# Kernel optimization log

Hardware: AMD Instinct MI355X
Metric: run time of the kernel (lower is better)

Reference implementation:

```python
import jax, jax.numpy as jnp
import numpy as np

B, L, D, H = 32, 512, 256, 4
A = 64
DH = D // H   # 64, item/pos head dim
AH = A // H   # 16, attribute head dim
EPS = 1e-12


def _split(t, h):
    # [B, L, d] -> [B, h, L, d//h]
    b, l, d = t.shape
    return t.reshape(b, l, h, d // h).transpose(0, 2, 1, 3)


def setup_inputs() -> dict:
    key = jax.random.key(0)
    ks = jax.random.split(key, 16)
    n = lambda k, s, sc=1.0: jax.random.normal(k, s, dtype=jnp.float32) * sc
    W = 0.02  # weight init scale
    return {
        "x": n(ks[0], (B, L, D)),
        "pos": n(ks[1], (B, L, D)),
        "true_item": n(ks[2], (B, L, D)),
        "attr0": n(ks[3], (B, L, 1, A)),
        "attr1": n(ks[4], (B, L, 1, A)),
        "mask": jnp.zeros((1, 1, L, L), jnp.float32),
        "Wq": n(ks[5], (D, D), W), "bq": jnp.zeros((D,), jnp.float32),
        "Wk": n(ks[6], (D, D), W), "bk": jnp.zeros((D,), jnp.float32),
        "Wqp": n(ks[7], (D, D), W), "bqp": jnp.zeros((D,), jnp.float32),
        "Wkp": n(ks[8], (D, D), W), "bkp": jnp.zeros((D,), jnp.float32),
        "Wq0": n(ks[9], (A, A), W), "bq0": jnp.zeros((A,), jnp.float32),
        "Wk0": n(ks[10], (A, A), W), "bk0": jnp.zeros((A,), jnp.float32),
        "Wq1": n(ks[11], (A, A), W), "bq1": jnp.zeros((A,), jnp.float32),
        "Wk1": n(ks[12], (A, A), W), "bk1": jnp.zeros((A,), jnp.float32),
        "Wd": n(ks[13], (D, D), W), "bd": jnp.zeros((D,), jnp.float32),
        "ln_g": jnp.ones((D,), jnp.float32),
        "ln_b": jnp.zeros((D,), jnp.float32),
    }


def reference(x, pos, true_item, attr0, attr1, mask,
              Wq, bq, Wk, bk, Wqp, bqp, Wkp, bkp,
              Wq0, bq0, Wk0, bk0, Wq1, bq1, Wk1, bk1,
              Wd, bd, ln_g, ln_b):
    lin = lambda t, W, b: t @ W + b
    # item / positional / attribute projections
    q = _split(lin(x, Wq, bq), H)           # [B,H,L,DH]
    k = _split(lin(x, Wk, bk), H)
    v = _split(true_item, H)                # value = true_item directly (no value proj in forward)
    qp = _split(lin(pos, Wqp, bqp), H)
    kp = _split(lin(pos, Wkp, bkp), H)
    a0 = attr0[:, :, 0, :]                  # squeeze(-2) -> [B,L,A]
    a1 = attr1[:, :, 0, :]
    q0 = _split(lin(a0, Wq0, bq0), H)       # [B,H,L,AH]
    k0 = _split(lin(a0, Wk0, bk0), H)
    q1 = _split(lin(a1, Wq1, bq1), H)
    k1 = _split(lin(a1, Wk1, bk1), H)
    # fused multi-source score accumulation (fusion_type='sum')
    scores = (jnp.einsum('bhld,bhmd->bhlm', q, k)
              + jnp.einsum('bhld,bhmd->bhlm', qp, kp)
              + jnp.einsum('bhld,bhmd->bhlm', q0, k0)
              + jnp.einsum('bhld,bhmd->bhlm', q1, k1))
    scores = scores / np.float32(np.sqrt(DH)) + mask
    probs = jax.nn.softmax(scores, axis=-1)  # attn_dropout p=0 -> identity
    ctx = jnp.einsum('bhlm,bhmd->bhld', probs, v)
    ctx = ctx.transpose(0, 2, 1, 3).reshape(B, L, D)
    h = lin(ctx, Wd, bd)                     # out_dropout p=0 -> identity
    mu = h.mean(-1, keepdims=True)
    var = h.var(-1, keepdims=True)
    return ln_g * (h - mu) / jnp.sqrt(var + EPS) + ln_b + x
```

## Files before the change

### kernel.cpp

```cpp
#include <hip/hip_runtime.h>

typedef unsigned short u16;
typedef unsigned int u32;

#define BB 32
#define LL 512
#define DD 256
#define HH 4
#define CAT 160
#define MTOT (BB*LL)

typedef __bf16 bf16x8 __attribute__((ext_vector_type(8)));
typedef float f32x4 __attribute__((ext_vector_type(4)));

__device__ __forceinline__ float b2f(u16 u) {
  union { u32 i; float f; } v; v.i = ((u32)u) << 16; return v.f;
}
__device__ __forceinline__ u16 f2b(float f) {
  union { float f; u32 i; } v; v.f = f;
  u32 x = v.i;
  u32 r = (x + 0x7FFFu + ((x >> 16) & 1u)) >> 16;
  return (u16)r;
}

template<bool F32>
__device__ __forceinline__ float ldin(const void* p, size_t i) {
  if constexpr (F32) return ((const float*)p)[i];
  else return b2f(((const u16*)p)[i]);
}

__device__ __forceinline__ bool f32mode(const void* lng) {
  return ((const u16*)lng)[0] == 0;
}

__device__ __forceinline__ f32x4 mfma_bf16(uint4 a, uint4 b, f32x4 c) {
  union U { uint4 u; bf16x8 v; };
  U ua, ub; ua.u = a; ub.u = b;
  return __builtin_amdgcn_mfma_f32_16x16x32_bf16(ua.v, ub.v, c, 0, 0, 0);
}

template<bool F32>
__device__ __forceinline__ void ld8(const void* p, size_t g, u16* tmp) {
  if constexpr (F32) {
    const float* gp = (const float*)p + g;
    float4 x0 = *(const float4*)gp;
    float4 x1 = *(const float4*)(gp + 4);
    tmp[0] = f2b(x0.x); tmp[1] = f2b(x0.y); tmp[2] = f2b(x0.z); tmp[3] = f2b(x0.w);
    tmp[4] = f2b(x1.x); tmp[5] = f2b(x1.y); tmp[6] = f2b(x1.z); tmp[7] = f2b(x1.w);
  } else {
    *(uint4*)tmp = *(const uint4*)((const u16*)p + g);
  }
}

struct WtOp { const void* W; u16* dst; int N; int K; };
struct WtArgs { WtOp ops[8]; const void* lng; };

template<bool F32>
__device__ void wtrans_body(const WtArgs& args, u16* T ) {
  WtOp op = args.ops[blockIdx.z];
  const int ntN = op.N >> 6;
  const int tx = blockIdx.x % ntN;
  const int ty = blockIdx.x / ntN;
  if (ty >= (op.K >> 6)) return;
  const int n0 = tx * 64, k0 = ty * 64;
  const int tid = threadIdx.x;
  for (int i = tid; i < 512; i += 256) {
    int r = i >> 3, c8 = (i & 7) * 8;
    u16 tmp[8];
    ld8<F32>(op.W, (size_t)(k0 + r) * op.N + n0 + c8, tmp);
    *(uint4*)&T[r * 72 + c8] = *(uint4*)tmp;
  }
  __syncthreads();
  for (int i = tid; i < 512; i += 256) {
    int n = i >> 3, k8 = (i & 7) * 8;
    u16 tmp[8];
#pragma unroll
    for (int j = 0; j < 8; ++j) tmp[j] = T[(k8 + j) * 72 + n];
    *(uint4*)(op.dst + (size_t)(n0 + n) * op.K + k0 + k8) = *(uint4*)tmp;
  }
}

__global__ __launch_bounds__(256) void wtrans_kernel(WtArgs args) {
  __shared__ __align__(16) u16 smem[64 * 72];
  if (f32mode(args.lng)) wtrans_body<true>(args, smem);
  else wtrans_body<false>(args, smem);
}

struct ProjOp {
  const void* X; const u16* Wt; const void* bias; u16* dst;
  int N; int K; int dstOff; int hShift; int dMask;
};
struct ProjArgs { ProjOp ops[8]; const void* lng; };

template<bool F32>
__device__ void proj_body(const ProjArgs& args, u16* smem) {
  ProjOp op = args.ops[blockIdx.z];
  const int n0g = blockIdx.y * 64;
  if (n0g >= op.N) return;
  const int m0 = blockIdx.x * 64;
  const int K = op.K;
  const int tid = threadIdx.x;
  const int wave = tid >> 6, lane = tid & 63;
  const int quad = lane >> 4, l15 = lane & 15;

  u16* Xs = smem;
  u16* Wt = smem + 64 * 136;

  f32x4 acc[4];
#pragma unroll
  for (int c = 0; c < 4; ++c) acc[c] = (f32x4){0.f, 0.f, 0.f, 0.f};

  for (int kc = 0; kc < K; kc += 128) {
    const int kw = (K - kc < 128) ? (K - kc) : 128;
    const int kw8 = kw >> 3;
    __syncthreads();
    for (int i = tid; i < 64 * kw8; i += 256) {
      int r = i / kw8, c8 = (i % kw8) * 8;
      u16 tmp[8];
      ld8<F32>(op.X, (size_t)(m0 + r) * K + kc + c8, tmp);
      *(uint4*)&Xs[r * 136 + c8] = *(uint4*)tmp;
    }
    for (int i = tid; i < 64 * kw8; i += 256) {
      int r = i / kw8, c8 = (i % kw8) * 8;
      *(uint4*)&Wt[r * 136 + c8] =
          *(const uint4*)(op.Wt + (size_t)(n0g + r) * K + kc + c8);
    }
    __syncthreads();
    const int nks = kw >> 5;
    for (int ks = 0; ks < nks; ++ks) {
      uint4 a = *(const uint4*)&Xs[(wave * 16 + l15) * 136 + ks * 32 + quad * 8];
#pragma unroll
      for (int c = 0; c < 4; ++c) {
        uint4 bb = *(const uint4*)&Wt[(c * 16 + l15) * 136 + ks * 32 + quad * 8];
        acc[c] = mfma_bf16(a, bb, acc[c]);
      }
    }
  }
  const int mrow = m0 + wave * 16 + quad * 4;
#pragma unroll
  for (int c = 0; c < 4; ++c) {
    int n = n0g + c * 16 + l15;
    int h = n >> op.hShift, d = n & op.dMask;
    float bias = ldin<F32>(op.bias, n);
#pragma unroll
    for (int r4 = 0; r4 < 4; ++r4) {
      int m = mrow + r4;
      int b = m >> 9, l = m & 511;
      op.dst[(size_t)((b * HH + h) * LL + l) * CAT + op.dstOff + d] =
          f2b(acc[c][r4] + bias);
    }
  }
}

__global__ __launch_bounds__(256) void proj_kernel(ProjArgs args) {
  __shared__ __align__(16) u16 smem[2 * 64 * 136];
  if (f32mode(args.lng)) proj_body<true>(args, smem);
  else proj_body<false>(args, smem);
}

template<bool F32>
__device__ void attn_body(
    const u16* __restrict__ qcat, const u16* __restrict__ kcat,
    const void* __restrict__ titm, const void* __restrict__ mask,
    float* __restrict__ ctx, u16* smem) {
  const int tid = threadIdx.x;
  const int wave = tid >> 6, lane = tid & 63;
  const int quad = lane >> 4, l15 = lane & 15;
  const int bh = blockIdx.x, b = bh >> 2, h = bh & 3;
  const int q0g = blockIdx.y * 64;

  u16* Ks = smem;
  u16* Vt = smem + 64 * 168;
  u16* Pw = smem + 64 * 168 + 64 * 72;

  for (int i = tid; i < 1280; i += 256) {
    int r = i / 20, c = (i % 20) * 8;
    *(uint4*)&Ks[r * 168 + c] =
        *(const uint4*)(qcat + (size_t)(bh * LL + q0g + r) * CAT + c);
  }
  __syncthreads();
  uint4 aq[5];
#pragma unroll
  for (int ks = 0; ks < 5; ++ks)
    aq[ks] = *(const uint4*)&Ks[(wave * 16 + l15) * 168 + ks * 32 + quad * 8];

  float lsum[4] = {0.f, 0.f, 0.f, 0.f};
  f32x4 oa[4];
#pragma unroll
  for (int vt = 0; vt < 4; ++vt) oa[vt] = (f32x4){0.f, 0.f, 0.f, 0.f};

  for (int c = 0; c < 8; ++c) {
    __syncthreads();
    for (int i = tid; i < 1280; i += 256) {
      int r = i / 20, col = (i % 20) * 8;
      *(uint4*)&Ks[r * 168 + col] =
          *(const uint4*)(kcat + (size_t)(bh * LL + c * 64 + r) * CAT + col);
    }
    for (int i = tid; i < 512; i += 256) {
      int t8 = i & 7, key = i >> 3;
      u16 tmp[8];
      ld8<F32>(titm, (size_t)(b * LL + c * 64 + key) * DD + h * 64 + t8 * 8, tmp);
#pragma unroll
      for (int j = 0; j < 8; ++j) Vt[(t8 * 8 + j) * 72 + key] = tmp[j];
    }
    __syncthreads();

    f32x4 s[4];
#pragma unroll
    for (int ct = 0; ct < 4; ++ct) {
      s[ct] = (f32x4){0.f, 0.f, 0.f, 0.f};
#pragma unroll
      for (int ks = 0; ks < 5; ++ks) {
        uint4 bk = *(const uint4*)&Ks[(ct * 16 + l15) * 168 + ks * 32 + quad * 8];
        s[ct] = mfma_bf16(aq[ks], bk, s[ct]);
      }
    }
#pragma unroll
    for (int ct = 0; ct < 4; ++ct) {
      int key = c * 64 + ct * 16 + l15;
#pragma unroll
      for (int r4 = 0; r4 < 4; ++r4) {
        int row = q0g + wave * 16 + quad * 4 + r4;
        float e = __expf(s[ct][r4] * 0.125f +
                         ldin<F32>(mask, (size_t)row * LL + key));
        lsum[r4] += e;
        Pw[wave * 16 * 72 + (quad * 4 + r4) * 72 + ct * 16 + l15] = f2b(e);
      }
    }
#pragma unroll
    for (int ks2 = 0; ks2 < 2; ++ks2) {
      uint4 pa = *(const uint4*)&Pw[wave * 16 * 72 + l15 * 72 + ks2 * 32 + quad * 8];
#pragma unroll
      for (int vt = 0; vt < 4; ++vt) {
        uint4 bb = *(const uint4*)&Vt[(vt * 16 + l15) * 72 + ks2 * 32 + quad * 8];
        oa[vt] = mfma_bf16(pa, bb, oa[vt]);
      }
    }
  }
  float inv[4];
#pragma unroll
  for (int r4 = 0; r4 < 4; ++r4) {
    for (int off = 1; off < 16; off <<= 1)
      lsum[r4] += __shfl_xor(lsum[r4], off);
    inv[r4] = 1.0f / lsum[r4];
  }
#pragma unroll
  for (int vt = 0; vt < 4; ++vt)
#pragma unroll
    for (int r4 = 0; r4 < 4; ++r4) {
      int row = q0g + wave * 16 + quad * 4 + r4;
      ctx[(size_t)(b * LL + row) * DD + h * 64 + vt * 16 + l15] =
          oa[vt][r4] * inv[r4];
    }
}

__global__ __launch_bounds__(256) void attn_kernel(
    const u16* __restrict__ qcat, const u16* __restrict__ kcat,
    const void* __restrict__ titm, const void* __restrict__ mask,
    float* __restrict__ ctx, const void* lng) {
  __shared__ __align__(16) u16 smem[64 * 168 + 64 * 72 + 4 * 16 * 72];
  if (f32mode(lng)) attn_body<true>(qcat, kcat, titm, mask, ctx, smem);
  else attn_body<false>(qcat, kcat, titm, mask, ctx, smem);
}

template<bool F32>
__device__ void outln_body(
    const float* __restrict__ ctx, const void* __restrict__ Wd,
    const void* __restrict__ bd, const void* __restrict__ ln_g,
    const void* __restrict__ ln_b, const void* __restrict__ x,
    float* __restrict__ out, float* smem) {
  const int tid = threadIdx.x;
  const int row0 = blockIdx.x * 8;
  float (*ctxs)[260] = (float (*)[260])smem;
  float* mu_s = smem + 8 * 260;
  float* rs_s = mu_s + 8;
  for (int i = tid; i < 8 * 256; i += 256) {
    int r = i >> 8, k = i & 255;
    ctxs[r][k] = ctx[(size_t)(row0 + r) * DD + k];
  }
  __syncthreads();
  const int n = tid;
  float acc[8];
  float bias = ldin<F32>(bd, n);
#pragma unroll
  for (int r = 0; r < 8; ++r) acc[r] = bias;
  for (int k4 = 0; k4 < 256; k4 += 4) {
    float w0 = ldin<F32>(Wd, (size_t)(k4 + 0) * DD + n);
    float w1 = ldin<F32>(Wd, (size_t)(k4 + 1) * DD + n);
    float w2 = ldin<F32>(Wd, (size_t)(k4 + 2) * DD + n);
    float w3 = ldin<F32>(Wd, (size_t)(k4 + 3) * DD + n);
#pragma unroll
    for (int r = 0; r < 8; ++r) {
      float4 c = *(const float4*)&ctxs[r][k4];
      acc[r] += c.x * w0 + c.y * w1 + c.z * w2 + c.w * w3;
    }
  }
  __syncthreads();
  float (*hs)[260] = ctxs;
#pragma unroll
  for (int r = 0; r < 8; ++r) hs[r][n] = acc[r];
  __syncthreads();
  {
    int w = tid >> 6, lane = tid & 63;
    for (int rr = 0; rr < 2; ++rr) {
      int r = w * 2 + rr;
      float v0 = hs[r][lane], v1 = hs[r][lane + 64];
      float v2 = hs[r][lane + 128], v3 = hs[r][lane + 192];
      float s = v0 + v1 + v2 + v3;
      for (int off = 1; off < 64; off <<= 1) s += __shfl_xor(s, off, 64);
      float mu = s * (1.0f / 256.0f);
      float d0 = v0 - mu, d1 = v1 - mu, d2 = v2 - mu, d3 = v3 - mu;
      float s2 = d0 * d0 + d1 * d1 + d2 * d2 + d3 * d3;
      for (int off = 1; off < 64; off <<= 1) s2 += __shfl_xor(s2, off, 64);
      if (lane == 0) {
        float var = fmaxf(s2 * (1.0f / 256.0f), 0.0f);
        mu_s[r] = mu;
        rs_s[r] = rsqrtf(var + 1e-12f);
      }
    }
  }
  __syncthreads();
  float g = ldin<F32>(ln_g, n), be = ldin<F32>(ln_b, n);
#pragma unroll
  for (int r = 0; r < 8; ++r) {
    size_t o = (size_t)(row0 + r) * DD + n;
    out[o] = g * (acc[r] - mu_s[r]) * rs_s[r] + be + ldin<F32>(x, o);
  }
}

__global__ __launch_bounds__(256) void outln_kernel(
    const float* __restrict__ ctx, const void* __restrict__ Wd,
    const void* __restrict__ bd, const void* __restrict__ ln_g,
    const void* __restrict__ ln_b, const void* __restrict__ x,
    float* __restrict__ out) {
  __shared__ __align__(16) float smem[8 * 260 + 16];
  if (f32mode(ln_g)) outln_body<true>(ctx, Wd, bd, ln_g, ln_b, x, out, smem);
  else outln_body<false>(ctx, Wd, bd, ln_g, ln_b, x, out, smem);
}

extern "C" void kernel_launch(void* const* d_in, const int* in_sizes, int n_in,
                              void* d_out, int out_size, void* d_ws, size_t ws_size,
                              hipStream_t stream) {
  const void* x    = d_in[0];
  const void* pos  = d_in[1];
  const void* titm = d_in[2];
  const void* at0  = d_in[3];
  const void* at1  = d_in[4];
  const void* mask = d_in[5];
  const void* Wq   = d_in[6];  const void* bq  = d_in[7];
  const void* Wk   = d_in[8];  const void* bk  = d_in[9];
  const void* Wqp  = d_in[10]; const void* bqp = d_in[11];
  const void* Wkp  = d_in[12]; const void* bkp = d_in[13];
  const void* Wq0  = d_in[14]; const void* bq0 = d_in[15];
  const void* Wk0  = d_in[16]; const void* bk0 = d_in[17];
  const void* Wq1  = d_in[18]; const void* bq1 = d_in[19];
  const void* Wk1  = d_in[20]; const void* bk1 = d_in[21];
  const void* Wd   = d_in[22]; const void* bd  = d_in[23];
  const void* lng  = d_in[24]; const void* lnb = d_in[25];
  float* out = (float*)d_out;

  u16* qcat = (u16*)d_ws;
  u16* kcat = qcat + (size_t)BB * HH * LL * CAT;
  u16* wt   = kcat + (size_t)BB * HH * LL * CAT;
  float* ctx = out;

  u16* wtD[4] = { wt, wt + 65536, wt + 131072, wt + 196608 };
  u16* wtA[4] = { wt + 262144, wt + 266240, wt + 270336, wt + 274432 };

  WtArgs wa;
  wa.ops[0] = { Wq,  wtD[0], 256, 256 };
  wa.ops[1] = { Wk,  wtD[1], 256, 256 };
  wa.ops[2] = { Wqp, wtD[2], 256, 256 };
  wa.ops[3] = { Wkp, wtD[3], 256, 256 };
  wa.ops[4] = { Wq0, wtA[0],  64,  64 };
  wa.ops[5] = { Wk0, wtA[1],  64,  64 };
  wa.ops[6] = { Wq1, wtA[2],  64,  64 };
  wa.ops[7] = { Wk1, wtA[3],  64,  64 };
  wa.lng = lng;

  ProjArgs pa;
  pa.ops[0] = { x,   wtD[0], bq,  qcat, 256, 256,   0, 6, 63 };
  pa.ops[1] = { x,   wtD[1], bk,  kcat, 256, 256,   0, 6, 63 };
  pa.ops[2] = { pos, wtD[2], bqp, qcat, 256, 256,  64, 6, 63 };
  pa.ops[3] = { pos, wtD[3], bkp, kcat, 256, 256,  64, 6, 63 };
  pa.ops[4] = { at0, wtA[0], bq0, qcat,  64,  64, 128, 4, 15 };
  pa.ops[5] = { at0, wtA[1], bk0, kcat,  64,  64, 128, 4, 15 };
  pa.ops[6] = { at1, wtA[2], bq1, qcat,  64,  64, 144, 4, 15 };
  pa.ops[7] = { at1, wtA[3], bk1, kcat,  64,  64, 144, 4, 15 };
  pa.lng = lng;

  hipLaunchKernelGGL(wtrans_kernel, dim3(16, 1, 8), dim3(256), 0, stream, wa);
  hipLaunchKernelGGL(proj_kernel, dim3(MTOT / 64, 4, 8), dim3(256), 0, stream, pa);
  hipLaunchKernelGGL(attn_kernel, dim3(BB * HH, LL / 64), dim3(256), 0, stream,
                     qcat, kcat, titm, mask, ctx, lng);
  hipLaunchKernelGGL(outln_kernel, dim3(MTOT / 8), dim3(256), 0, stream,
                     ctx, Wd, bd, lng, lnb, x, out);
}
```

Measured before the change: 281.5 us.

## Use bf16 MFMA for output projection with fused LayerNorm epilogue

The output dense layer plus LayerNorm, previously a scalar fp32 FMA loop over 8 rows per block, becomes a 64-row-tile bf16 MFMA GEMM. Wd is pre-transposed into bf16 by an added op in the weight-transpose kernel. LayerNorm statistics are computed from register accumulators with cross-lane shuffles, using a single-pass E[x^2]-mu^2 variance. The goal is to cut the fp32 ALU cost and the repeated weight reads. In exchange, ctx is rounded to bf16 before the projection, which adds numerical error.

```diff
diff --git a/kernel.cpp b/kernel.cpp
--- a/kernel.cpp
+++ b/kernel.cpp
@@ -53,7 +53,7 @@
 }
 
 struct WtOp { const void* W; u16* dst; int N; int K; };
-struct WtArgs { WtOp ops[8]; const void* lng; };
+struct WtArgs { WtOp ops[9]; const void* lng; };
 
 template<bool F32>
 __device__ void wtrans_body(const WtArgs& args, u16* T ) {
@@ -265,77 +265,95 @@
 
 template<bool F32>
 __device__ void outln_body(
-    const float* __restrict__ ctx, const void* __restrict__ Wd,
+    const float* __restrict__ ctx, const u16* __restrict__ wdt,
     const void* __restrict__ bd, const void* __restrict__ ln_g,
     const void* __restrict__ ln_b, const void* __restrict__ x,
-    float* __restrict__ out, float* smem) {
+    float* __restrict__ out, u16* smem) {
   const int tid = threadIdx.x;
-  const int row0 = blockIdx.x * 8;
-  float (*ctxs)[260] = (float (*)[260])smem;
-  float* mu_s = smem + 8 * 260;
-  float* rs_s = mu_s + 8;
-  for (int i = tid; i < 8 * 256; i += 256) {
-    int r = i >> 8, k = i & 255;
-    ctxs[r][k] = ctx[(size_t)(row0 + r) * DD + k];
-  }
-  __syncthreads();
-  const int n = tid;
-  float acc[8];
-  float bias = ldin<F32>(bd, n);
-#pragma unroll
-  for (int r = 0; r < 8; ++r) acc[r] = bias;
-  for (int k4 = 0; k4 < 256; k4 += 4) {
-    float w0 = ldin<F32>(Wd, (size_t)(k4 + 0) * DD + n);
-    float w1 = ldin<F32>(Wd, (size_t)(k4 + 1) * DD + n);
-    float w2 = ldin<F32>(Wd, (size_t)(k4 + 2) * DD + n);
-    float w3 = ldin<F32>(Wd, (size_t)(k4 + 3) * DD + n);
-#pragma unroll
-    for (int r = 0; r < 8; ++r) {
-      float4 c = *(const float4*)&ctxs[r][k4];
-      acc[r] += c.x * w0 + c.y * w1 + c.z * w2 + c.w * w3;
-    }
-  }
-  __syncthreads();
-  float (*hs)[260] = ctxs;
-#pragma unroll
-  for (int r = 0; r < 8; ++r) hs[r][n] = acc[r];
-  __syncthreads();
-  {
-    int w = tid >> 6, lane = tid & 63;
-    for (int rr = 0; rr < 2; ++rr) {
-      int r = w * 2 + rr;
-      float v0 = hs[r][lane], v1 = hs[r][lane + 64];
-      float v2 = hs[r][lane + 128], v3 = hs[r][lane + 192];
-      float s = v0 + v1 + v2 + v3;
-      for (int off = 1; off < 64; off <<= 1) s += __shfl_xor(s, off, 64);
-      float mu = s * (1.0f / 256.0f);
-      float d0 = v0 - mu, d1 = v1 - mu, d2 = v2 - mu, d3 = v3 - mu;
-      float s2 = d0 * d0 + d1 * d1 + d2 * d2 + d3 * d3;
-      for (int off = 1; off < 64; off <<= 1) s2 += __shfl_xor(s2, off, 64);
-      if (lane == 0) {
-        float var = fmaxf(s2 * (1.0f / 256.0f), 0.0f);
-        mu_s[r] = mu;
-        rs_s[r] = rsqrtf(var + 1e-12f);
+  const int wave = tid >> 6, lane = tid & 63;
+  const int quad = lane >> 4, l15 = lane & 15;
+  const int m0 = blockIdx.x * 64;
+
+  u16* Cs = smem;
+  u16* Ws = smem + 64 * 72;
+
+  f32x4 acc[16];
+#pragma unroll
+  for (int nt = 0; nt < 16; ++nt) acc[nt] = (f32x4){0.f, 0.f, 0.f, 0.f};
+
+  for (int kc = 0; kc < 256; kc += 64) {
+    __syncthreads();
+    for (int i = tid; i < 512; i += 256) {
+      int r = i >> 3, c8 = (i & 7) * 8;
+      const float* gp = ctx + (size_t)(m0 + r) * DD + kc + c8;
+      float4 x0 = *(const float4*)gp;
+      float4 x1 = *(const float4*)(gp + 4);
+      u16 tmp[8];
+      tmp[0] = f2b(x0.x); tmp[1] = f2b(x0.y); tmp[2] = f2b(x0.z); tmp[3] = f2b(x0.w);
+      tmp[4] = f2b(x1.x); tmp[5] = f2b(x1.y); tmp[6] = f2b(x1.z); tmp[7] = f2b(x1.w);
+      *(uint4*)&Cs[r * 72 + c8] = *(uint4*)tmp;
+    }
+    for (int i = tid; i < 2048; i += 256) {
+      int n = i >> 3, k8 = (i & 7) * 8;
+      *(uint4*)&Ws[n * 72 + k8] =
+          *(const uint4*)(wdt + (size_t)n * DD + kc + k8);
+    }
+    __syncthreads();
+#pragma unroll
+    for (int ks = 0; ks < 2; ++ks) {
+      uint4 a = *(const uint4*)&Cs[(wave * 16 + l15) * 72 + ks * 32 + quad * 8];
+#pragma unroll
+      for (int nt = 0; nt < 16; ++nt) {
+        uint4 bb = *(const uint4*)&Ws[(nt * 16 + l15) * 72 + ks * 32 + quad * 8];
+        acc[nt] = mfma_bf16(a, bb, acc[nt]);
       }
     }
   }
-  __syncthreads();
-  float g = ldin<F32>(ln_g, n), be = ldin<F32>(ln_b, n);
-#pragma unroll
-  for (int r = 0; r < 8; ++r) {
-    size_t o = (size_t)(row0 + r) * DD + n;
-    out[o] = g * (acc[r] - mu_s[r]) * rs_s[r] + be + ldin<F32>(x, o);
+#pragma unroll
+  for (int nt = 0; nt < 16; ++nt) {
+    float bdv = ldin<F32>(bd, nt * 16 + l15);
+#pragma unroll
+    for (int r4 = 0; r4 < 4; ++r4) acc[nt][r4] += bdv;
+  }
+  float mu[4], rsig[4];
+#pragma unroll
+  for (int r4 = 0; r4 < 4; ++r4) {
+    float s = 0.f, s2 = 0.f;
+#pragma unroll
+    for (int nt = 0; nt < 16; ++nt) {
+      float v = acc[nt][r4];
+      s += v; s2 += v * v;
+    }
+    for (int off = 1; off < 16; off <<= 1) {
+      s += __shfl_xor(s, off);
+      s2 += __shfl_xor(s2, off);
+    }
+    float m = s * (1.0f / 256.0f);
+    float var = fmaxf(s2 * (1.0f / 256.0f) - m * m, 0.0f);
+    mu[r4] = m;
+    rsig[r4] = rsqrtf(var + 1e-12f);
+  }
+#pragma unroll
+  for (int nt = 0; nt < 16; ++nt) {
+    int n = nt * 16 + l15;
+    float g = ldin<F32>(ln_g, n), be = ldin<F32>(ln_b, n);
+#pragma unroll
+    for (int r4 = 0; r4 < 4; ++r4) {
+      int m = m0 + wave * 16 + quad * 4 + r4;
+      size_t o = (size_t)m * DD + n;
+      out[o] = g * (acc[nt][r4] - mu[r4]) * rsig[r4] + be + ldin<F32>(x, o);
+    }
   }
 }
 
 __global__ __launch_bounds__(256) void outln_kernel(
-    const float* __restrict__ ctx, const void* __restrict__ Wd,
+    const float* __restrict__ ctx, const u16* __restrict__ wdt,
     const void* __restrict__ bd, const void* __restrict__ ln_g,
     const void* __restrict__ ln_b, const void* __restrict__ x,
     float* __restrict__ out) {
-  __shared__ __align__(16) float smem[8 * 260 + 16];
-  if (f32mode(ln_g)) outln_body<true>(ctx, Wd, bd, ln_g, ln_b, x, out, smem);
-  else outln_body<false>(ctx, Wd, bd, ln_g, ln_b, x, out, smem);
+  __shared__ __align__(16) u16 smem[64 * 72 + 256 * 72];
+  if (f32mode(ln_g)) outln_body<true>(ctx, wdt, bd, ln_g, ln_b, x, out, smem);
+  else outln_body<false>(ctx, wdt, bd, ln_g, ln_b, x, out, smem);
 }
 
 extern "C" void kernel_launch(void* const* d_in, const int* in_sizes, int n_in,
@@ -366,6 +384,7 @@
 
   u16* wtD[4] = { wt, wt + 65536, wt + 131072, wt + 196608 };
   u16* wtA[4] = { wt + 262144, wt + 266240, wt + 270336, wt + 274432 };
+  u16* wtWd  = wt + 278528;
 
   WtArgs wa;
   wa.ops[0] = { Wq,  wtD[0], 256, 256 };
@@ -376,6 +395,7 @@
   wa.ops[5] = { Wk0, wtA[1],  64,  64 };
   wa.ops[6] = { Wq1, wtA[2],  64,  64 };
   wa.ops[7] = { Wk1, wtA[3],  64,  64 };
+  wa.ops[8] = { Wd,  wtWd,  256, 256 };
   wa.lng = lng;
 
   ProjArgs pa;
@@ -389,10 +409,10 @@
   pa.ops[7] = { at1, wtA[3], bk1, kcat,  64,  64, 144, 4, 15 };
   pa.lng = lng;
 
-  hipLaunchKernelGGL(wtrans_kernel, dim3(16, 1, 8), dim3(256), 0, stream, wa);
+  hipLaunchKernelGGL(wtrans_kernel, dim3(16, 1, 9), dim3(256), 0, stream, wa);
   hipLaunchKernelGGL(proj_kernel, dim3(MTOT / 64, 4, 8), dim3(256), 0, stream, pa);
   hipLaunchKernelGGL(attn_kernel, dim3(BB * HH, LL / 64), dim3(256), 0, stream,
                      qcat, kcat, titm, mask, ctx, lng);
-  hipLaunchKernelGGL(outln_kernel, dim3(MTOT / 8), dim3(256), 0, stream,
-                     ctx, Wd, bd, lng, lnb, x, out);
-}
+  hipLaunchKernelGGL(outln_kernel, dim3(MTOT / 64), dim3(256), 0, stream,
+                     ctx, wtWd, bd, lng, lnb, x, out);
+}
```

After: 242.0 us. -14.0%, faster.
